# Performance work log

Hardware: AMD Instinct MI355X
Metric: run time of the kernel (lower is better)

Reference implementation:

```python
import jax, jax.numpy as jnp
import numpy as np

NUM_HEADS = 32
NUM_KV_HEADS = 8
HEAD_DIM = 128
WINDOW = 512
NUM_META = 4


def _swa_sink_mask(S):
    # allowed = causal & (within sliding window OR sink/meta token)
    i = jnp.arange(S)[:, None]   # q_idx
    j = jnp.arange(S)[None, :]   # kv_idx
    return (i >= j) & (((i - j) <= WINDOW) | (j < NUM_META))


def setup_inputs() -> dict:
    key = jax.random.key(0)
    k1, k2, k3 = jax.random.split(key, 3)
    B, S = 1, 2048
    return {
        "query_states": jax.random.normal(k1, (B, S, NUM_HEADS * HEAD_DIM), dtype=jnp.float32),
        "key_states": jax.random.normal(k2, (B, S, NUM_KV_HEADS * HEAD_DIM), dtype=jnp.float32),
        "value_states": jax.random.normal(k3, (B, S, NUM_KV_HEADS * HEAD_DIM), dtype=jnp.float32),
    }


def reference(query_states, key_states, value_states):
    B, S, _ = query_states.shape
    n_rep = NUM_HEADS // NUM_KV_HEADS
    # [B, H, S, D]
    q = query_states.reshape(B, S, NUM_HEADS, HEAD_DIM).transpose(0, 2, 1, 3)
    k = key_states.reshape(B, S, NUM_KV_HEADS, HEAD_DIM).transpose(0, 2, 1, 3)
    v = value_states.reshape(B, S, NUM_KV_HEADS, HEAD_DIM).transpose(0, 2, 1, 3)
    # repeat_kv: interleaved repeat along head dim (GQA)
    k = jnp.repeat(k, n_rep, axis=1)
    v = jnp.repeat(v, n_rep, axis=1)

    scale = 1.0 / jnp.sqrt(jnp.float32(HEAD_DIM))  # flex_attention default scale
    scores = jnp.einsum("bhqd,bhkd->bhqk", q, k) * scale
    mask = _swa_sink_mask(S)  # [S, S], every row has q_idx==kv_idx allowed
    scores = jnp.where(mask[None, None], scores, -jnp.inf)
    attn = jax.nn.softmax(scores, axis=-1)
    out = jnp.einsum("bhqk,bhkd->bhqd", attn, v)
    return out.transpose(0, 2, 1, 3).reshape(B, S, NUM_HEADS * HEAD_DIM)
```

## Files before the change

### kernel.cpp

```cpp
#include <hip/hip_runtime.h>
#include <math.h>

typedef __attribute__((ext_vector_type(8))) short bf16x8;
typedef __attribute__((ext_vector_type(16))) float f32x16;

#define WIN 512
#define META 4
#define QSCALE (0.08838834764831845f * 1.4426950408889634f)
#define MFIX2 20.197730572445487f

union U8 { int4 i4; bf16x8 bf; };

static __device__ __forceinline__ unsigned bf16_rne(float x) {
  unsigned u = __float_as_uint(x);
  return (u + 0x7FFFu + ((u >> 16) & 1u)) >> 16;
}
static __device__ __forceinline__ unsigned pk2_rne(float a, float b) {
  return bf16_rne(a) | (bf16_rne(b) << 16);
}
static __device__ __forceinline__ unsigned pk2_tr(float a, float b) {
  return (__float_as_uint(a) >> 16) | (__float_as_uint(b) & 0xFFFF0000u);
}
static __device__ __forceinline__ void gload16(const void* g, void* l) {
  __builtin_amdgcn_global_load_lds(
      (const __attribute__((address_space(1))) unsigned int*)g,
      (__attribute__((address_space(3))) unsigned int*)l, 16, 0, 0);
}

__global__ __launch_bounds__(256) void swa_prep(
    const float* __restrict__ Kg, const float* __restrict__ Vg,
    unsigned short* __restrict__ Kw, unsigned short* __restrict__ Vw)
{
  __shared__ float Kf[64][132];
  __shared__ float Vf[64][132];
  const int tid = threadIdx.x;
  const int hk = blockIdx.x & 7, tj = blockIdx.x >> 3;
  const int j0 = tj * 64;
  const int krow = tid >> 5;
  const int f4c = tid & 31;
  #pragma unroll
  for (int r = 0; r < 8; ++r) {
    const int key = r * 8 + krow;
    *(float4*)&Kf[key][f4c * 4] =
        *(const float4*)(Kg + (size_t)(j0 + key) * 1024 + hk * 128 + f4c * 4);
    *(float4*)&Vf[key][f4c * 4] =
        *(const float4*)(Vg + (size_t)(j0 + key) * 1024 + hk * 128 + f4c * 4);
  }
  __syncthreads();
  unsigned short* kout = Kw + ((size_t)(hk * 32 + tj)) * 8192;
  #pragma unroll
  for (int p = 0; p < 4; ++p) {
    const int gid = p * 256 + tid;
    const int s = gid >> 6, key = gid & 63;
    const float* src = &Kf[key][s * 8];
    *(int4*)(kout + gid * 8) = make_int4(
        (int)pk2_tr(src[0], src[1]), (int)pk2_tr(src[2], src[3]),
        (int)pk2_tr(src[4], src[5]), (int)pk2_tr(src[6], src[7]));
  }
  unsigned short* vout = Vw + ((size_t)(hk * 32 + tj)) * 8192;
  #pragma unroll
  for (int p = 0; p < 4; ++p) {
    const int fid = p * 256 + tid;
    const int c = fid >> 7, dim = fid & 127;
    const int kb = 16 * (c >> 1) + 4 * (c & 1);
    *(int4*)(vout + fid * 8) = make_int4(
        (int)pk2_tr(Vf[kb + 0][dim], Vf[kb + 1][dim]),
        (int)pk2_tr(Vf[kb + 2][dim], Vf[kb + 3][dim]),
        (int)pk2_tr(Vf[kb + 8][dim], Vf[kb + 9][dim]),
        (int)pk2_tr(Vf[kb + 10][dim], Vf[kb + 11][dim]));
  }
}

__global__ __launch_bounds__(256, 4) void swa_fused(
    const float* __restrict__ Qg, const unsigned short* __restrict__ Kw,
    const unsigned short* __restrict__ Vw, float* __restrict__ Og)
{
  __shared__ __align__(16) unsigned short KsB[2][4096];
  __shared__ __align__(16) unsigned short VtB[2][2048];

  const int tid = threadIdx.x;
  const int lane = tid & 63, wid = tid >> 6;
  const int cl = lane & 31, hl = lane >> 5;
  const int bid = blockIdx.x;
  const int hk = bid & 7;
  const int rest = bid >> 3;
  const int qt = rest >> 1;
  const int dh = rest & 1;
  const int q0t = qt << 5;
  const int h = hk * 4 + wid;

  int4 qf[8];
  {
    const float* qrow = Qg + (size_t)(q0t + cl) * 4096 + h * 128 + hl * 8;
    #pragma unroll
    for (int kc = 0; kc < 8; ++kc) {
      float4 x = *(const float4*)(qrow + kc * 16);
      float4 y = *(const float4*)(qrow + kc * 16 + 4);
      qf[kc] = make_int4(pk2_rne(x.x*QSCALE, x.y*QSCALE), pk2_rne(x.z*QSCALE, x.w*QSCALE),
                         pk2_rne(y.x*QSCALE, y.y*QSCALE), pk2_rne(y.z*QSCALE, y.w*QSCALE));
    }
  }

  f32x16 acc[2];
  #pragma unroll
  for (int nt = 0; nt < 2; ++nt)
    #pragma unroll
    for (int i = 0; i < 16; ++i) acc[nt][i] = 0.f;
  float lp = 0.f;

  const int jstart = (q0t > WIN) ? (q0t - WIN) : 0;
  const int sink = (jstart > 0) ? 1 : 0;
  const int niter = ((q0t + 31 - jstart) >> 5) + 1 + sink;

  auto stage = [&](const int j, unsigned short* kd, unsigned short* vd) {
    const size_t tbase = ((size_t)(hk * 32 + (j >> 6))) << 14;
    const int half64 = (j >> 5) & 1;
    const char* ksrc = (const char*)Kw + tbase + half64 * 512 + (tid >> 5) * 1024 + (tid & 31) * 16;
    gload16(ksrc, (char*)kd + tid * 16);
    gload16(ksrc + 8 * 1024, (char*)kd + 4096 + tid * 16);
    const char* vsrc = (const char*)Vw + tbase + half64 * 8192 +
                       (tid >> 6) * 2048 + (64 * dh + (tid & 63)) * 16;
    gload16(vsrc, (char*)vd + tid * 16);
  };

  stage(sink ? 0 : jstart, KsB[0], VtB[0]);
  __syncthreads();

  for (int t = 0; t < niter; ++t) {
    const int jts = (sink && t == 0) ? 0 : jstart + ((t - sink) << 5);
    const int cb = t & 1;
    const unsigned short* kCur = KsB[cb];
    const unsigned short* vCur = VtB[cb];

    if (t + 1 < niter)
      stage(jstart + ((t + 1 - sink) << 5), KsB[cb ^ 1], VtB[cb ^ 1]);

    f32x16 sv;
    #pragma unroll
    for (int i = 0; i < 16; ++i) sv[i] = 0.f;
    __builtin_amdgcn_s_setprio(1);
    #pragma unroll
    for (int kc = 0; kc < 8; ++kc) {
      U8 b; b.i4 = qf[kc];
      U8 a; a.i4 = *(const int4*)(kCur + (2 * kc + hl) * 256 + cl * 8);
      sv = __builtin_amdgcn_mfma_f32_32x32x16_bf16(a.bf, b.bf, sv, 0, 0, 0);
    }
    __builtin_amdgcn_s_setprio(0);

    const bool needMask = (jts + 31 > q0t) || (q0t + 31 - jts > WIN);
    unsigned pk[8];
    const int q = q0t + cl;
    #pragma unroll
    for (int ri = 0; ri < 16; ri += 2) {
      const int koff = (ri & 3) + 8 * (ri >> 2) + 4 * hl;
      bool okE = true, okO = true;
      if (needMask) {
        const int kE = jts + koff;
        okE = (q >= kE)     && (((q - kE)     <= WIN) || (kE     < META));
        okO = (q >= kE + 1) && (((q - kE - 1) <= WIN) || (kE + 1 < META));
      }
      unsigned uE = okE ? (__float_as_uint(__builtin_amdgcn_exp2f(sv[ri]   - MFIX2)) & 0xFFFF0000u) : 0u;
      unsigned uO = okO ? (__float_as_uint(__builtin_amdgcn_exp2f(sv[ri+1] - MFIX2)) & 0xFFFF0000u) : 0u;
      lp += __uint_as_float(uE) + __uint_as_float(uO);
      pk[ri >> 1] = __builtin_amdgcn_perm(uO, uE, 0x07060302u);
    }

    __builtin_amdgcn_s_setprio(1);
    {
      U8 a0; a0.i4 = make_int4((int)pk[0], (int)pk[1], (int)pk[2], (int)pk[3]);
      #pragma unroll
      for (int nt2 = 0; nt2 < 2; ++nt2) {
        U8 b; b.i4 = *(const int4*)(vCur + hl * 512 + (nt2 * 32 + cl) * 8);
        acc[nt2] = __builtin_amdgcn_mfma_f32_32x32x16_bf16(a0.bf, b.bf, acc[nt2], 0, 0, 0);
      }
      U8 a1; a1.i4 = make_int4((int)pk[4], (int)pk[5], (int)pk[6], (int)pk[7]);
      #pragma unroll
      for (int nt2 = 0; nt2 < 2; ++nt2) {
        U8 b; b.i4 = *(const int4*)(vCur + (2 + hl) * 512 + (nt2 * 32 + cl) * 8);
        acc[nt2] = __builtin_amdgcn_mfma_f32_32x32x16_bf16(a1.bf, b.bf, acc[nt2], 0, 0, 0);
      }
    }
    __builtin_amdgcn_s_setprio(0);

    __syncthreads();
  }

  const float ltot = lp + __shfl_xor(lp, 32);
  const float inv = __fdividef(1.0f, ltot);
  #pragma unroll
  for (int ri = 0; ri < 16; ++ri) {
    const int rl = (ri & 3) + 8 * (ri >> 2) + 4 * hl;
    const float invq = __shfl(inv, rl, 64);
    #pragma unroll
    for (int nt2 = 0; nt2 < 2; ++nt2) {
      Og[(size_t)(q0t + rl) * 4096 + h * 128 + dh * 64 + nt2 * 32 + cl] =
          acc[nt2][ri] * invq;
    }
  }
}

extern "C" void kernel_launch(void* const* d_in, const int* in_sizes, int n_in,
                              void* d_out, int out_size, void* d_ws, size_t ws_size,
                              hipStream_t stream) {
  const float* Q = (const float*)d_in[0];
  const float* K = (const float*)d_in[1];
  const float* V = (const float*)d_in[2];
  float* O = (float*)d_out;
  unsigned short* Kw = (unsigned short*)d_ws;
  unsigned short* Vw = Kw + (size_t)8 * 32 * 8192;
  hipLaunchKernelGGL(swa_prep, dim3(256), dim3(256), 0, stream, K, V, Kw, Vw);
  hipLaunchKernelGGL(swa_fused, dim3(1024), dim3(256), 0, stream, Q, Kw, Vw, O);
}
```

Baseline: 127.5 us.

## Enlarge attention tiles to 64 queries by 128 keys and read V directly from global

Each block now covers 64 query rows with 8 waves and the full head dimension, no longer splitting it in two. Keys are staged in 128-key double-buffered LDS tiles, and 32-key subtiles that fall entirely outside the window are skipped. V fragments are read straight from global memory instead of LDS. This removes the redundant QK^T work the head-dim split caused and cuts the number of barriers, at the cost of more accumulator registers, lower occupancy, and uncached global V loads on the critical path.

```diff
diff --git a/kernel.cpp b/kernel.cpp
--- a/kernel.cpp
+++ b/kernel.cpp
@@ -71,27 +71,25 @@
   }
 }
 
-__global__ __launch_bounds__(256, 4) void swa_fused(
+__global__ __launch_bounds__(512, 2) void swa_fused(
     const float* __restrict__ Qg, const unsigned short* __restrict__ Kw,
     const unsigned short* __restrict__ Vw, float* __restrict__ Og)
 {
-  __shared__ __align__(16) unsigned short KsB[2][4096];
-  __shared__ __align__(16) unsigned short VtB[2][2048];
+  __shared__ __align__(16) unsigned short KsB[2][16384];
 
   const int tid = threadIdx.x;
   const int lane = tid & 63, wid = tid >> 6;
   const int cl = lane & 31, hl = lane >> 5;
   const int bid = blockIdx.x;
   const int hk = bid & 7;
-  const int rest = bid >> 3;
-  const int qt = rest >> 1;
-  const int dh = rest & 1;
-  const int q0t = qt << 5;
-  const int h = hk * 4 + wid;
+  const int bq = bid >> 3;
+  const int q0 = bq << 6;
+  const int h = hk * 4 + (wid & 3);
+  const int qw0 = q0 + ((wid >> 2) << 5);
 
   int4 qf[8];
   {
-    const float* qrow = Qg + (size_t)(q0t + cl) * 4096 + h * 128 + hl * 8;
+    const float* qrow = Qg + (size_t)(qw0 + cl) * 4096 + h * 128 + hl * 8;
     #pragma unroll
     for (int kc = 0; kc < 8; ++kc) {
       float4 x = *(const float4*)(qrow + kc * 16);
@@ -101,40 +99,30 @@
     }
   }
 
-  f32x16 acc[2];
-  #pragma unroll
-  for (int nt = 0; nt < 2; ++nt)
+  f32x16 acc[4];
+  #pragma unroll
+  for (int nt = 0; nt < 4; ++nt)
     #pragma unroll
     for (int i = 0; i < 16; ++i) acc[nt][i] = 0.f;
-  float lp = 0.f;
-
-  const int jstart = (q0t > WIN) ? (q0t - WIN) : 0;
+  float lpA = 0.f, lpB = 0.f;
+
+  const int jstart = (q0 > WIN) ? ((q0 - WIN) & ~127) : 0;
   const int sink = (jstart > 0) ? 1 : 0;
-  const int niter = ((q0t + 31 - jstart) >> 5) + 1 + sink;
-
-  auto stage = [&](const int j, unsigned short* kd, unsigned short* vd) {
-    const size_t tbase = ((size_t)(hk * 32 + (j >> 6))) << 14;
-    const int half64 = (j >> 5) & 1;
-    const char* ksrc = (const char*)Kw + tbase + half64 * 512 + (tid >> 5) * 1024 + (tid & 31) * 16;
-    gload16(ksrc, (char*)kd + tid * 16);
-    gload16(ksrc + 8 * 1024, (char*)kd + 4096 + tid * 16);
-    const char* vsrc = (const char*)Vw + tbase + half64 * 8192 +
-                       (tid >> 6) * 2048 + (64 * dh + (tid & 63)) * 16;
-    gload16(vsrc, (char*)vd + tid * 16);
+  const int niter = ((q0 + 63 - jstart) >> 7) + 1 + sink;
+
+  auto stageK = [&](const int j, unsigned short* kd) {
+    const int tj64 = j >> 6;
+    #pragma unroll
+    for (int h2 = 0; h2 < 2; ++h2) {
+      const char* src = (const char*)Kw + (((size_t)(hk * 32 + tj64 + h2)) << 14) + tid * 16;
+      char* dst = (char*)kd + h2 * 16384 + tid * 16;
+      gload16(src, dst);
+      gload16(src + 8192, dst + 8192);
+    }
   };
 
-  stage(sink ? 0 : jstart, KsB[0], VtB[0]);
-  __syncthreads();
-
-  for (int t = 0; t < niter; ++t) {
-    const int jts = (sink && t == 0) ? 0 : jstart + ((t - sink) << 5);
-    const int cb = t & 1;
-    const unsigned short* kCur = KsB[cb];
-    const unsigned short* vCur = VtB[cb];
-
-    if (t + 1 < niter)
-      stage(jstart + ((t + 1 - sink) << 5), KsB[cb ^ 1], VtB[cb ^ 1]);
-
+  auto subtile = [&](const unsigned short* kb, const int jts, const size_t vbsh,
+                     const bool fm, float& lp) {
     f32x16 sv;
     #pragma unroll
     for (int i = 0; i < 16; ++i) sv[i] = 0.f;
@@ -142,14 +130,14 @@
     #pragma unroll
     for (int kc = 0; kc < 8; ++kc) {
       U8 b; b.i4 = qf[kc];
-      U8 a; a.i4 = *(const int4*)(kCur + (2 * kc + hl) * 256 + cl * 8);
+      U8 a; a.i4 = *(const int4*)(kb + (2 * kc + hl) * 512 + cl * 8);
       sv = __builtin_amdgcn_mfma_f32_32x32x16_bf16(a.bf, b.bf, sv, 0, 0, 0);
     }
     __builtin_amdgcn_s_setprio(0);
 
-    const bool needMask = (jts + 31 > q0t) || (q0t + 31 - jts > WIN);
+    const bool needMask = fm || (jts + 31 > qw0) || (qw0 + 31 - jts > WIN);
     unsigned pk[8];
-    const int q = q0t + cl;
+    const int q = qw0 + cl;
     #pragma unroll
     for (int ri = 0; ri < 16; ri += 2) {
       const int koff = (ri & 3) + 8 * (ri >> 2) + 4 * hl;
@@ -166,25 +154,56 @@
     }
 
     __builtin_amdgcn_s_setprio(1);
+    const unsigned short* vb = Vw + vbsh;
     {
       U8 a0; a0.i4 = make_int4((int)pk[0], (int)pk[1], (int)pk[2], (int)pk[3]);
       #pragma unroll
-      for (int nt2 = 0; nt2 < 2; ++nt2) {
-        U8 b; b.i4 = *(const int4*)(vCur + hl * 512 + (nt2 * 32 + cl) * 8);
-        acc[nt2] = __builtin_amdgcn_mfma_f32_32x32x16_bf16(a0.bf, b.bf, acc[nt2], 0, 0, 0);
+      for (int nt = 0; nt < 4; ++nt) {
+        U8 b; b.i4 = *(const int4*)(vb + hl * 1024 + (nt * 32 + cl) * 8);
+        acc[nt] = __builtin_amdgcn_mfma_f32_32x32x16_bf16(a0.bf, b.bf, acc[nt], 0, 0, 0);
       }
       U8 a1; a1.i4 = make_int4((int)pk[4], (int)pk[5], (int)pk[6], (int)pk[7]);
       #pragma unroll
-      for (int nt2 = 0; nt2 < 2; ++nt2) {
-        U8 b; b.i4 = *(const int4*)(vCur + (2 + hl) * 512 + (nt2 * 32 + cl) * 8);
-        acc[nt2] = __builtin_amdgcn_mfma_f32_32x32x16_bf16(a1.bf, b.bf, acc[nt2], 0, 0, 0);
+      for (int nt = 0; nt < 4; ++nt) {
+        U8 b; b.i4 = *(const int4*)(vb + (2 + hl) * 1024 + (nt * 32 + cl) * 8);
+        acc[nt] = __builtin_amdgcn_mfma_f32_32x32x16_bf16(a1.bf, b.bf, acc[nt], 0, 0, 0);
       }
     }
     __builtin_amdgcn_s_setprio(0);
+  };
+
+  stageK(sink ? 0 : jstart, KsB[0]);
+  __syncthreads();
+
+  for (int t = 0; t < niter; ++t) {
+    const bool isSink = (sink != 0) && (t == 0);
+    const int jt = isSink ? 0 : jstart + ((t - sink) << 7);
+    const int cb = t & 1;
+
+    if (t + 1 < niter)
+      stageK(jstart + ((t + 1 - sink) << 7), KsB[cb ^ 1]);
+
+    if (isSink) {
+      subtile(&KsB[cb][0], 0, ((size_t)(hk * 32)) * 8192, true, lpA);
+    } else {
+      const int tj64 = jt >> 6;
+      #pragma unroll
+      for (int st = 0; st < 4; ++st) {
+        const int jts = jt + (st << 5);
+        const bool above = (jts > qw0 + 31);
+        const bool below = (jts + 31 < qw0 - WIN) && (jts >= META);
+        if (!above && !below) {
+          subtile(&KsB[cb][(st >> 1) * 8192 + (st & 1) * 256], jts,
+                  ((size_t)(hk * 32 + tj64 + (st >> 1))) * 8192 + (size_t)(st & 1) * 4096,
+                  false, (st & 1) ? lpB : lpA);
+        }
+      }
+    }
 
     __syncthreads();
   }
 
+  const float lp = lpA + lpB;
   const float ltot = lp + __shfl_xor(lp, 32);
   const float inv = __fdividef(1.0f, ltot);
   #pragma unroll
@@ -192,9 +211,8 @@
     const int rl = (ri & 3) + 8 * (ri >> 2) + 4 * hl;
     const float invq = __shfl(inv, rl, 64);
     #pragma unroll
-    for (int nt2 = 0; nt2 < 2; ++nt2) {
-      Og[(size_t)(q0t + rl) * 4096 + h * 128 + dh * 64 + nt2 * 32 + cl] =
-          acc[nt2][ri] * invq;
+    for (int nt = 0; nt < 4; ++nt) {
+      Og[(size_t)(qw0 + rl) * 4096 + h * 128 + nt * 32 + cl] = acc[nt][ri] * invq;
     }
   }
 }
@@ -209,5 +227,5 @@
   unsigned short* Kw = (unsigned short*)d_ws;
   unsigned short* Vw = Kw + (size_t)8 * 32 * 8192;
   hipLaunchKernelGGL(swa_prep, dim3(256), dim3(256), 0, stream, K, V, Kw, Vw);
-  hipLaunchKernelGGL(swa_fused, dim3(1024), dim3(256), 0, stream, Q, Kw, Vw, O);
-}
+  hipLaunchKernelGGL(swa_fused, dim3(256), dim3(512), 0, stream, Q, Kw, Vw, O);
+}
```

Measured after the change: 131.8 us. +3.4%, slower.
